# Performance work log

Hardware: AMD Instinct MI355X
Metric: run time of the kernel (lower is better)

Reference implementation:

```python
import jax, jax.numpy as jnp
import numpy as np

B, L = 4, 2048
D_MODEL, D_INNER, D_STATE, DT_RANK, K = 512, 1024, 16, 64, 4


def setup_inputs() -> dict:
    key = jax.random.key(0)
    ks = jax.random.split(key, 21)
    def n(k, shape, s=0.02):
        return (jax.random.normal(k, shape) * s).astype(jnp.float32)
    inp = {"x": jax.random.normal(ks[0], (B, L, D_MODEL), jnp.float32)}
    for i, sfx in enumerate(("f", "b")):
        o = 1 + i * 8
        inp[f"W_in_{sfx}"] = n(ks[o], (2 * D_INNER, D_MODEL))
        inp[f"conv_w_{sfx}"] = n(ks[o + 1], (D_INNER, 1, K), 0.1)
        inp[f"conv_b_{sfx}"] = jnp.zeros((D_INNER,), jnp.float32)
        inp[f"A_log_{sfx}"] = (jax.random.normal(ks[o + 2], (D_STATE, D_INNER)) * 0.1).astype(jnp.float32)
        inp[f"D_{sfx}"] = jnp.ones((D_INNER,), jnp.float32)
        inp[f"Wx_{sfx}"] = n(ks[o + 3], (DT_RANK + 2 * D_STATE, D_INNER))
        inp[f"Wdt_{sfx}"] = n(ks[o + 4], (D_INNER, DT_RANK), DT_RANK ** -0.5)
        dt = jnp.exp(jax.random.uniform(ks[o + 5], (D_INNER,)) * (np.log(0.1) - np.log(0.001)) + np.log(0.001))
        inp[f"bdt_{sfx}"] = (dt + jnp.log(-jnp.expm1(-dt))).astype(jnp.float32)
        inp[f"Wout_{sfx}"] = n(ks[o + 6], (D_MODEL, D_INNER))
    return inp


def _mamba_block(x, W_in, conv_w, conv_b, A_log, Dp, Wx, Wdt, bdt, Wout):
    # x: [B, L, d_model]
    xz = jnp.einsum('bld,ed->ble', x, W_in)              # [B, L, 2*d_inner]
    xb, zb = xz[..., :D_INNER], xz[..., D_INNER:]
    # causal depthwise conv over time
    xc = jnp.transpose(xb, (0, 2, 1))                     # [B, M, L]
    xc = jax.lax.conv_general_dilated(
        xc, conv_w, window_strides=(1,), padding=[(K - 1, 0)],
        feature_group_count=D_INNER,
        dimension_numbers=('NCH', 'OIH', 'NCH')) + conv_b[None, :, None]
    xb = jax.nn.silu(jnp.transpose(xc, (0, 2, 1)))        # [B, L, M]
    # input-dependent SSM parameters
    proj = jnp.einsum('blm,pm->blp', xb, Wx)              # [B, L, dt_rank+2D]
    dt_in = proj[..., :DT_RANK]
    Bs = proj[..., DT_RANK:DT_RANK + D_STATE]             # [B, L, D]
    Cs = proj[..., DT_RANK + D_STATE:]                    # [B, L, D]
    dt = jax.nn.softplus(jnp.einsum('blr,mr->blm', dt_in, Wdt) + bdt)  # [B, L, M]
    A_T = -jnp.exp(A_log).T                               # [M, D]

    def step(h, inp):
        dt_t, x_t, B_t, C_t = inp                         # [B,M],[B,M],[B,D],[B,D]
        dA = jnp.exp(dt_t[:, :, None] * A_T[None])        # [B, M, D]
        h = dA * h + (dt_t * x_t)[:, :, None] * B_t[:, None, :]
        y_t = jnp.einsum('bmd,bd->bm', h, C_t)
        return h, y_t

    xs = (jnp.moveaxis(dt, 1, 0), jnp.moveaxis(xb, 1, 0),
          jnp.moveaxis(Bs, 1, 0), jnp.moveaxis(Cs, 1, 0))
    h0 = jnp.zeros((x.shape[0], D_INNER, D_STATE), x.dtype)
    _, ys = jax.lax.scan(step, h0, xs)                    # [L, B, M]
    y = jnp.moveaxis(ys, 0, 1) + Dp * xb                  # [B, L, M]
    y = y * jax.nn.silu(zb)                               # SiLU gate
    return jnp.einsum('blm,dm->bld', y, Wout)             # [B, L, d_model]


def reference(x,
              W_in_f, conv_w_f, conv_b_f, A_log_f, D_f, Wx_f, Wdt_f, bdt_f, Wout_f,
              W_in_b, conv_w_b, conv_b_b, A_log_b, D_b, Wx_b, Wdt_b, bdt_b, Wout_b):
    out_f = _mamba_block(x, W_in_f, conv_w_f, conv_b_f, A_log_f, D_f, Wx_f, Wdt_f, bdt_f, Wout_f)
    out_b = jnp.flip(_mamba_block(jnp.flip(x, 1), W_in_b, conv_w_b, conv_b_b, A_log_b, D_b, Wx_b, Wdt_b, bdt_b, Wout_b), 1)
    return out_f + out_b
```

## Files before the change

### kernel.cpp

```cpp
#include <hip/hip_runtime.h>
#include <hip/hip_bf16.h>
#include <cstdint>
#include <cstdio>

typedef float f32x4 __attribute__((ext_vector_type(4)));
typedef float f32x2 __attribute__((ext_vector_type(2)));
typedef short s16x8 __attribute__((ext_vector_type(8)));
typedef unsigned int u32x2 __attribute__((ext_vector_type(2)));

__device__ __forceinline__ float us2f(unsigned short u){
  union { unsigned int i; float f; } v; v.i = ((unsigned int)u) << 16; return v.f;
}
__device__ __forceinline__ unsigned short f2us(float f){
  union { float f; unsigned int i; } v; v.f = f;
  unsigned int r = v.i + 0x7fffu + ((v.i >> 16) & 1u);
  return (unsigned short)(r >> 16);
}
__device__ __forceinline__ void gload_lds16(const void* g, void* l){
  __builtin_amdgcn_global_load_lds(
      (const __attribute__((address_space(1))) unsigned int*)g,
      (__attribute__((address_space(3))) unsigned int*)l, 16, 0, 0);
}

#define PK0 0.999962f

__global__ __launch_bounds__(256)
void prep_k(const float* __restrict__ x,
            const float* __restrict__ W_in_f, const float* __restrict__ W_in_b,
            const float* __restrict__ Wx_f,   const float* __restrict__ Wx_b,
            const float* __restrict__ Wdt_f,  const float* __restrict__ Wdt_b,
            const float* __restrict__ Wout_f, const float* __restrict__ Wout_b,
            const float* __restrict__ Alog_f, const float* __restrict__ Alog_b,
            const float* __restrict__ bdt_f,  const float* __restrict__ bdt_b,
            unsigned short* __restrict__ W1cat, unsigned short* __restrict__ Wxpad,
            unsigned short* __restrict__ Wdtb,  unsigned short* __restrict__ Woutcat,
            float* __restrict__ A2, float* __restrict__ bdtcat,
            unsigned short* __restrict__ xbf, float* __restrict__ Cf)
{
  long i = (long)blockIdx.x * 256 + threadIdx.x;
  if (i < 4194304) {
    xbf[i] = f2us(x[i]); return;
  }
  i -= 4194304;
  if (i < 2097152) {
    int n = (int)(i >> 9), k = (int)(i & 511);
    float v = (n < 2048) ? W_in_f[(long)n*512 + k] : W_in_b[(long)(n-2048)*512 + k];
    W1cat[i] = f2us(v); return;
  }
  i -= 2097152;
  if (i < 262144) {
    int dir = (int)(i >> 17); long r = i & 131071; int n = (int)(r >> 10), k = (int)(r & 1023);
    const float* Wx = dir ? Wx_b : Wx_f;
    Wxpad[(long)dir*131072 + r] = f2us(n < 96 ? Wx[(long)n*1024 + k] : 0.f); return;
  }
  i -= 262144;
  if (i < 131072) {
    int dir = (int)(i >> 16); long r = i & 65535;
    Wdtb[i] = f2us((dir ? Wdt_b : Wdt_f)[r]); return;
  }
  i -= 131072;
  if (i < 1048576) {
    int n = (int)(i >> 11), k = (int)(i & 2047);
    float v = (k < 1024) ? Wout_f[(long)n*1024 + k] : Wout_b[(long)n*1024 + (k-1024)];
    Woutcat[i] = f2us(v); return;
  }
  i -= 1048576;
  if (i < 32768) {
    int dir = (int)(i >> 14); long r = i & 16383; int m = (int)(r >> 4), d = (int)(r & 15);
    const float* Al = dir ? Alog_b : Alog_f;
    A2[i] = -__expf(Al[(long)d*1024 + m]) * 1.4426950408889634f; return;
  }
  i -= 32768;
  if (i < 2048) {
    int dir = (int)(i >> 10), m = (int)(i & 1023);
    bdtcat[i] = (dir ? bdt_b : bdt_f)[m]; return;
  }
  i -= 2048;
  if (i < 98304) {
    int dir = (int)(i / 49152); long r = i % 49152;
    int m = (int)(r / 48), j = (int)(r % 48);
    int k = j >> 4, d = j & 15;
    const float* Al = dir ? Alog_b : Alog_f;
    const float w = -__expf(Al[(long)d*1024 + m]);
    float c;
    if (k == 0)      c = 0.999150f * w;
    else if (k == 1) c = 0.492809f * w * w;
    else             c = 0.139212f * w * w * w;
    Cf[(long)dir*49152 + (long)m*48 + (k << 4) + d] = c;
    return;
  }
}

template<int OUT_MODE>
__global__ __launch_bounds__(256)
void gemm_bt(const unsigned short* __restrict__ Ap, const unsigned short* __restrict__ Bp,
             void* __restrict__ Cp, const float* __restrict__ biasp,
             float* __restrict__ bcf,
             int K, int lda, int ldb, int ldc,
             long az, long bz, long cz, int biasz)
{
  const int z   = blockIdx.z;
  const int tid = threadIdx.x;
  const int bm  = blockIdx.x, bn = blockIdx.y;

  __shared__ __align__(16) unsigned short Ash[128][32];
  __shared__ __align__(16) unsigned short Bsh[128][32];

  const int wave = tid >> 6, lane = tid & 63;
  const int wr = (wave >> 1) << 6, wc = (wave & 1) << 6;
  const int fr = lane & 15, fs = lane >> 4;

  const int r0 = tid >> 2;
  const int sg = tid & 3, kofs = sg << 3;

  const unsigned short* Ag = Ap + (long)z * az;
  const unsigned short* Bg = Bp + (long)z * bz;

  const long aoff0 = (long)(bm*128 + r0)*lda + kofs;
  const long aoff1 = aoff0 + (long)64*lda;
  const long boff0 = (long)(bn*128 + r0)*ldb + kofs;
  const long boff1 = boff0 + (long)64*ldb;

  unsigned short* lA0 = &Ash[r0][kofs];
  unsigned short* lA1 = &Ash[64 + r0][kofs];
  unsigned short* lB0 = &Bsh[r0][kofs];
  unsigned short* lB1 = &Bsh[64 + r0][kofs];

  f32x4 acc[4][4];
  #pragma unroll
  for (int i=0;i<4;i++)
    #pragma unroll
    for (int j=0;j<4;j++) acc[i][j] = (f32x4){0.f,0.f,0.f,0.f};

  const int NK = K >> 5;
  for (int ks = 0; ks < NK; ++ks){
    const long k0 = (long)ks << 5;
    __syncthreads();
    gload_lds16(Ag + aoff0 + k0, lA0);
    gload_lds16(Ag + aoff1 + k0, lA1);
    gload_lds16(Bg + boff0 + k0, lB0);
    gload_lds16(Bg + boff1 + k0, lB1);
    __syncthreads();

    s16x8 af[4], bfv[4];
    #pragma unroll
    for (int i=0;i<4;i++){
      af[i]  = *(const s16x8*)&Ash[wr + i*16 + fr][fs << 3];
      bfv[i] = *(const s16x8*)&Bsh[wc + i*16 + fr][fs << 3];
    }
    #pragma unroll
    for (int i=0;i<4;i++)
      #pragma unroll
      for (int j=0;j<4;j++)
        acc[i][j] = __builtin_amdgcn_mfma_f32_16x16x32_bf16(bfv[j], af[i], acc[i][j], 0, 0, 0);
  }

  #pragma unroll
  for (int i=0;i<4;i++){
    const int row = bm*128 + wr + i*16 + fr;
    #pragma unroll
    for (int j=0;j<4;j++){
      const int c0 = bn*128 + wc + j*16 + (fs << 2);
      f32x4 v = acc[i][j];
      const long cbase = (long)z*cz + (long)row*ldc + c0;
      if (OUT_MODE == 2){
        *(f32x4*)((float*)Cp + cbase) = v;
      } else if (OUT_MODE == 1){
        const f32x4 b4 = *(const f32x4*)(biasp + z*biasz + c0);
        u32x2 o;
        unsigned short s[4];
        #pragma unroll
        for (int e=0;e<4;e++){
          float t = v[e] + b4[e];
          t = fmaxf(t, 0.f) + log1pf(__expf(-fabsf(t)));
          s[e] = f2us(t);
        }
        o[0] = (unsigned int)s[0] | ((unsigned int)s[1] << 16);
        o[1] = (unsigned int)s[2] | ((unsigned int)s[3] << 16);
        *(u32x2*)((unsigned short*)Cp + cbase) = o;
      } else {
        u32x2 o;
        o[0] = (unsigned int)f2us(v[0]) | ((unsigned int)f2us(v[1]) << 16);
        o[1] = (unsigned int)f2us(v[2]) | ((unsigned int)f2us(v[3]) << 16);
        *(u32x2*)((unsigned short*)Cp + cbase) = o;
        if (OUT_MODE == 3 && c0 >= 64 && c0 < 96){
          *(f32x4*)(bcf + ((long)z*8192 + row)*32 + (c0 - 64)) = v;
        }
      }
    }
  }
}

__global__ __launch_bounds__(256)
void conv_silu_k(const unsigned short* __restrict__ xz,
                 const float* __restrict__ wf, const float* __restrict__ cbf,
                 const float* __restrict__ wb, const float* __restrict__ cbb,
                 unsigned short* __restrict__ xbc)
{
  const int tid = threadIdx.x;
  const long tok = blockIdx.x;
  const int l   = (int)(tok & 2047);
  const int dir = tid >> 7;
  const int mg  = (tid & 127) << 3;
  const float* w  = dir ? wb  : wf;
  const float* cb = dir ? cbb : cbf;
  const long rowb = tok << 12;
  const int  xcol = (dir << 11) + mg;

  f32x4 wv[8];
  #pragma unroll
  for (int e=0;e<8;e++) wv[e] = *(const f32x4*)(w + (mg + e)*4);
  const f32x4 cb0 = *(const f32x4*)(cb + mg);
  const f32x4 cb1 = *(const f32x4*)(cb + mg + 4);

  float acc[8];
  #pragma unroll
  for (int e=0;e<4;e++){ acc[e]=cb0[e]; acc[4+e]=cb1[e]; }

  #pragma unroll
  for (int k=0;k<4;k++){
    const int off = dir ? (3 - k) : (k - 3);
    const int pos = l + off;
    if (pos >= 0 && pos < 2048){
      const s16x8 xv = *(const s16x8*)(xz + rowb + ((long)off << 12) + xcol);
      #pragma unroll
      for (int e=0;e<8;e++)
        acc[e] = __builtin_fmaf(wv[e][k], us2f((unsigned short)xv[e]), acc[e]);
    }
  }
  s16x8 out;
  #pragma unroll
  for (int e=0;e<8;e++){
    const float s = acc[e] / (1.f + __expf(-acc[e]));
    out[e] = (short)f2us(s);
  }
  *(s16x8*)(xbc + tok*2048 + (dir << 10) + mg) = out;
}

#define SCHUNK 32
#define NCHUNK 64

__global__ __launch_bounds__(256)
void scan1_k(const unsigned short* __restrict__ dtb, const unsigned short* __restrict__ xbc,
             const float* __restrict__ BCf, const float* __restrict__ Cf,
             unsigned short* __restrict__ hloc, float* __restrict__ Ssum)
{
  const int tidx = threadIdx.x;
  const int cb = blockIdx.x, c = blockIdx.y, bz = blockIdx.z;
  const int b = bz >> 1, dir = bz & 1;
  const int m = cb*256 + tidx;

  float C1[16], C2[16], C3[16];
  { const f32x4* p = (const f32x4*)(Cf + ((long)dir*1024 + m)*48);
    #pragma unroll
    for (int q=0;q<4;q++){
      f32x4 v1=p[q], v2=p[q+4], v3=p[q+8];
      #pragma unroll
      for (int e=0;e<4;e++){ C1[q*4+e]=v1[e]; C2[q*4+e]=v2[e]; C3[q*4+e]=v3[e]; } } }

  const int  l0 = dir ? (2047 - c*SCHUNK) : (c*SCHUNK);
  const int  ls = dir ? -1 : 1;
  const long tok0 = (long)b*2048 + l0;
  const unsigned short* dtp = dtb + (((long)dir) << 23) + tok0*1024 + m;
  const unsigned short* xvp = xbc + tok0*2048 + (dir << 10) + m;
  const float* bcp = BCf + ((long)dir*8192 + tok0)*32;
  const long dstp = (long)ls*1024, xstp = (long)ls*2048, bstp = (long)ls*32;

  float h[16];
  #pragma unroll
  for (int d=0;d<16;d++) h[d]=0.f;
  float S = 0.f;

  unsigned short du = *dtp, xu = *xvp;
  for (int t=0;t<SCHUNK;t++){
    const float dt = us2f(du), xv = us2f(xu);
    dtp += dstp; xvp += xstp;
    du = *dtp; xu = *xvp;
    S += dt;
    const float u = dt * xv;
    const float dt2 = dt*dt, dt3 = dt2*dt;
    const f32x4 bv0 = *(const f32x4*)(bcp);
    const f32x4 bv1 = *(const f32x4*)(bcp + 4);
    const f32x4 bv2 = *(const f32x4*)(bcp + 8);
    const f32x4 bv3 = *(const f32x4*)(bcp + 12);
    bcp += bstp;
    #pragma unroll
    for (int d=0;d<16;d++){
      const float bval = (d<4)? bv0[d&3] : (d<8)? bv1[d&3] : (d<12)? bv2[d&3] : bv3[d&3];
      float a = __builtin_fmaf(C1[d], dt, PK0);
      a = __builtin_fmaf(C2[d], dt2, a);
      a = __builtin_fmaf(C3[d], dt3, a);
      h[d] = __builtin_fmaf(a, h[d], u * bval);
    }
  }
  const long o = (((long)bz * NCHUNK) + c)*1024 + m;
  s16x8 hv0, hv1;
  #pragma unroll
  for (int e=0;e<8;e++){ hv0[e] = (short)f2us(h[e]); hv1[e] = (short)f2us(h[8+e]); }
  *(s16x8*)(hloc + (o << 4))     = hv0;
  *(s16x8*)(hloc + (o << 4) + 8) = hv1;
  Ssum[o] = S;
}

__global__ __launch_bounds__(256)
void scan2_k(const float* __restrict__ A2, const float* __restrict__ Ssum,
             unsigned short* __restrict__ hloc)
{
  const long idx = (long)blockIdx.x*256 + threadIdx.x;
  const long bz = idx >> 14; const int r = (int)(idx & 16383);
  const int dir = (int)(bz & 1);
  const float a2 = A2[((long)dir << 14) + r];
  const long base = bz * NCHUNK;
  float hs = 0.f;
  float hlN = us2f(hloc[base*16384 + r]);
  float SN  = Ssum[base*1024 + (r >> 4)];
  for (int c=0;c<NCHUNK;c++){
    const float hl = hlN, Sv = SN;
    const int cn = (c+1 < NCHUNK) ? c+1 : c;
    hlN = us2f(hloc[(base+cn)*16384 + r]);
    SN  = Ssum[(base+cn)*1024 + (r >> 4)];
    const float P = __builtin_amdgcn_exp2f(a2 * Sv);
    hloc[(base+c)*16384 + r] = f2us(hs);
    hs = __builtin_fmaf(P, hs, hl);
  }
}

__global__ __launch_bounds__(256)
void scan3_k(const unsigned short* __restrict__ dtb, const unsigned short* __restrict__ xbc,
             const float* __restrict__ BCf, const float* __restrict__ Cf,
             const unsigned short* __restrict__ hstart, const unsigned short* __restrict__ xz,
             const float* __restrict__ D_f, const float* __restrict__ D_b,
             unsigned short* __restrict__ ybuf)
{
  const int tidx = threadIdx.x;
  const int cb = blockIdx.x, c = blockIdx.y, bz = blockIdx.z;
  const int b = bz >> 1, dir = bz & 1;
  const int m = cb*256 + tidx;

  float C1[16], C2[16], C3[16];
  { const f32x4* p = (const f32x4*)(Cf + ((long)dir*1024 + m)*48);
    #pragma unroll
    for (int q=0;q<4;q++){
      f32x4 v1=p[q], v2=p[q+4], v3=p[q+8];
      #pragma unroll
      for (int e=0;e<4;e++){ C1[q*4+e]=v1[e]; C2[q*4+e]=v2[e]; C3[q*4+e]=v3[e]; } } }
  const float Dm = (dir ? D_b : D_f)[m];

  float h[16];
  { const long o = ((((long)bz*NCHUNK) + c)*1024 + m) << 4;
    s16x8 hv0 = *(const s16x8*)(hstart + o);
    s16x8 hv1 = *(const s16x8*)(hstart + o + 8);
    #pragma unroll
    for (int e=0;e<8;e++){ h[e] = us2f((unsigned short)hv0[e]);
                           h[8+e] = us2f((unsigned short)hv1[e]); } }

  const int  l0 = dir ? (2047 - c*SCHUNK) : (c*SCHUNK);
  const int  ls = dir ? -1 : 1;
  const long tok0 = (long)b*2048 + l0;
  const unsigned short* dtp = dtb + (((long)dir) << 23) + tok0*1024 + m;
  const unsigned short* xvp = xbc + tok0*2048 + (dir << 10) + m;
  const unsigned short* zp  = xz  + (tok0 << 12) + (dir << 11) + 1024 + m;
  unsigned short*       yp  = ybuf + tok0*2048 + (dir << 10) + m;
  const float* bcp = BCf + ((long)dir*8192 + tok0)*32;
  const long dstp = (long)ls*1024, xstp = (long)ls*2048, zstp = (long)ls << 12;
  const long bstp = (long)ls*32;

  unsigned short du = *dtp, xu = *xvp, zu = *zp;
  for (int t=0;t<SCHUNK;t++){
    const float dt = us2f(du), xv = us2f(xu), zb = us2f(zu);
    dtp += dstp; xvp += xstp; zp += zstp;
    du = *dtp; xu = *xvp; zu = *zp;
    const float u = dt * xv;
    const float dt2 = dt*dt, dt3 = dt2*dt;
    const f32x4 bv0 = *(const f32x4*)(bcp);
    const f32x4 bv1 = *(const f32x4*)(bcp + 4);
    const f32x4 bv2 = *(const f32x4*)(bcp + 8);
    const f32x4 bv3 = *(const f32x4*)(bcp + 12);
    const f32x4 cv0 = *(const f32x4*)(bcp + 16);
    const f32x4 cv1 = *(const f32x4*)(bcp + 20);
    const f32x4 cv2 = *(const f32x4*)(bcp + 24);
    const f32x4 cv3 = *(const f32x4*)(bcp + 28);
    bcp += bstp;
    float y0=0.f, y1=0.f;
    #pragma unroll
    for (int d=0;d<16;d++){
      const float bval = (d<4)? bv0[d&3] : (d<8)? bv1[d&3] : (d<12)? bv2[d&3] : bv3[d&3];
      const float cval = (d<4)? cv0[d&3] : (d<8)? cv1[d&3] : (d<12)? cv2[d&3] : cv3[d&3];
      float a = __builtin_fmaf(C1[d], dt, PK0);
      a = __builtin_fmaf(C2[d], dt2, a);
      a = __builtin_fmaf(C3[d], dt3, a);
      h[d] = __builtin_fmaf(a, h[d], u * bval);
      if (d & 1) y1 = __builtin_fmaf(h[d], cval, y1);
      else       y0 = __builtin_fmaf(h[d], cval, y0);
    }
    const float y = (y0 + y1) + Dm * xv;
    const float gate = zb / (1.f + __expf(-zb));
    *yp = f2us(y * gate);
    yp += xstp;
  }
}

extern "C" void kernel_launch(void* const* d_in, const int* in_sizes, int n_in,
                              void* d_out, int out_size, void* d_ws, size_t ws_size,
                              hipStream_t stream)
{
  const float* x      = (const float*)d_in[0];
  const float* W_in_f = (const float*)d_in[1];
  const float* convw_f= (const float*)d_in[2];
  const float* convb_f= (const float*)d_in[3];
  const float* Alog_f = (const float*)d_in[4];
  const float* D_f    = (const float*)d_in[5];
  const float* Wx_f   = (const float*)d_in[6];
  const float* Wdt_f  = (const float*)d_in[7];
  const float* bdt_f  = (const float*)d_in[8];
  const float* Wout_f = (const float*)d_in[9];
  const float* W_in_b = (const float*)d_in[10];
  const float* convw_b= (const float*)d_in[11];
  const float* convb_b= (const float*)d_in[12];
  const float* Alog_b = (const float*)d_in[13];
  const float* D_b    = (const float*)d_in[14];
  const float* Wx_b   = (const float*)d_in[15];
  const float* Wdt_b  = (const float*)d_in[16];
  const float* bdt_b  = (const float*)d_in[17];
  const float* Wout_b = (const float*)d_in[18];

  char* w = (char*)d_ws;
  auto carve = [&](size_t bytes) -> char* {
    char* p = w; w += (bytes + 255) & ~(size_t)255; return p;
  };
  unsigned short* W1cat   = (unsigned short*)carve(4096ULL*512*2);
  unsigned short* Wxpad   = (unsigned short*)carve(2ULL*128*1024*2);
  unsigned short* Wdtb    = (unsigned short*)carve(2ULL*1024*64*2);
  unsigned short* Woutcat = (unsigned short*)carve(512ULL*2048*2);
  float*          A2      = (float*)carve(2ULL*1024*16*4);
  float*          bdtcat  = (float*)carve(2048ULL*4);
  float*          Cf      = (float*)carve(2ULL*1024*48*4);
  float*          BCf     = (float*)carve(2ULL*8192*32*4);
  unsigned short* xz      = (unsigned short*)carve(8192ULL*4096*2);
  unsigned short* xbc     = (unsigned short*)carve(8192ULL*2048*2);
  unsigned short* proj    = (unsigned short*)carve(2ULL*8192*128*2);
  unsigned short* dtb     = (unsigned short*)carve(2ULL*8192*1024*2);
  unsigned short* ybuf    = (unsigned short*)carve(8192ULL*2048*2);
  unsigned short* hloc    = (unsigned short*)carve(8ULL*NCHUNK*1024*16*2);
  float*          Ssum    = (float*)carve(8ULL*NCHUNK*1024*4);
  unsigned short* xbf     = ybuf;

  if ((size_t)(w - (char*)d_ws) > ws_size) {
    fprintf(stderr, "kernel_launch: ws too small (%zu needed, %zu given)\n",
            (size_t)(w - (char*)d_ws), ws_size);
    return;
  }

  prep_k<<<dim3(30728), 256, 0, stream>>>(x, W_in_f, W_in_b, Wx_f, Wx_b, Wdt_f, Wdt_b,
                                          Wout_f, Wout_b, Alog_f, Alog_b, bdt_f, bdt_b,
                                          W1cat, Wxpad, Wdtb, Woutcat, A2, bdtcat, xbf, Cf);
  gemm_bt<0><<<dim3(64,32,1), 256, 0, stream>>>(xbf, W1cat, xz, nullptr, nullptr,
                                                512, 512, 512, 4096, 0, 0, 0, 0);
  conv_silu_k<<<dim3(8192), 256, 0, stream>>>(xz, convw_f, convb_f, convw_b, convb_b, xbc);
  gemm_bt<3><<<dim3(64,1,2), 256, 0, stream>>>(xbc, Wxpad, proj, nullptr, BCf,
                                               1024, 2048, 1024, 128,
                                               1024, 131072, 1048576, 0);
  gemm_bt<1><<<dim3(64,8,2), 256, 0, stream>>>(proj, Wdtb, dtb, bdtcat, nullptr,
                                               64, 128, 64, 1024,
                                               1048576, 65536, 8388608, 1024);
  scan1_k<<<dim3(4,NCHUNK,8), 256, 0, stream>>>(dtb, xbc, BCf, Cf, hloc, Ssum);
  scan2_k<<<dim3(512), 256, 0, stream>>>(A2, Ssum, hloc);
  scan3_k<<<dim3(4,NCHUNK,8), 256, 0, stream>>>(dtb, xbc, BCf, Cf, hloc, xz, D_f, D_b, ybuf);
  gemm_bt<2><<<dim3(64,4,1), 256, 0, stream>>>(ybuf, Woutcat, d_out, nullptr, nullptr,
                                               2048, 2048, 2048, 512, 0, 0, 0, 0);
}
```

Before: 348.8 us.

## Double GEMM K-tile to 64 and XOR-swizzle LDS layout

The bf16 GEMM now loads a 64-wide K slice per iteration instead of 32, which halves the number of barrier pairs per K loop and issues two MFMA sub-steps between barriers. The global source column is XOR-swizzled by row so that the LDS fragment reads are spread across banks and avoid conflicts. In exchange it doubles LDS use per block, which may lower occupancy, and it requires K to be a multiple of 64.

Result: faster. 322.7 us (-7.5%).

```diff
diff --git a/kernel.cpp b/kernel.cpp
--- a/kernel.cpp
+++ b/kernel.cpp
@@ -103,28 +103,24 @@
   const int tid = threadIdx.x;
   const int bm  = blockIdx.x, bn = blockIdx.y;
 
-  __shared__ __align__(16) unsigned short Ash[128][32];
-  __shared__ __align__(16) unsigned short Bsh[128][32];
+  __shared__ __align__(16) unsigned short Ash[128][64];
+  __shared__ __align__(16) unsigned short Bsh[128][64];
 
   const int wave = tid >> 6, lane = tid & 63;
   const int wr = (wave >> 1) << 6, wc = (wave & 1) << 6;
   const int fr = lane & 15, fs = lane >> 4;
 
-  const int r0 = tid >> 2;
-  const int sg = tid & 3, kofs = sg << 3;
+  const int rr  = tid >> 3;
+  const int csp = tid & 7;
+  const int csg = ((csp ^ (rr & 7)) << 3);
 
   const unsigned short* Ag = Ap + (long)z * az;
   const unsigned short* Bg = Bp + (long)z * bz;
 
-  const long aoff0 = (long)(bm*128 + r0)*lda + kofs;
-  const long aoff1 = aoff0 + (long)64*lda;
-  const long boff0 = (long)(bn*128 + r0)*ldb + kofs;
-  const long boff1 = boff0 + (long)64*ldb;
-
-  unsigned short* lA0 = &Ash[r0][kofs];
-  unsigned short* lA1 = &Ash[64 + r0][kofs];
-  unsigned short* lB0 = &Bsh[r0][kofs];
-  unsigned short* lB1 = &Bsh[64 + r0][kofs];
+  const long abase = (long)(bm*128 + rr)*lda + csg;
+  const long bbase = (long)(bn*128 + rr)*ldb + csg;
+  unsigned short* lA = &Ash[rr][csp << 3];
+  unsigned short* lB = &Bsh[rr][csp << 3];
 
   f32x4 acc[4][4];
   #pragma unroll
@@ -132,27 +128,33 @@
     #pragma unroll
     for (int j=0;j<4;j++) acc[i][j] = (f32x4){0.f,0.f,0.f,0.f};
 
-  const int NK = K >> 5;
+  const int NK = K >> 6;
   for (int ks = 0; ks < NK; ++ks){
-    const long k0 = (long)ks << 5;
+    const long k0 = (long)ks << 6;
     __syncthreads();
-    gload_lds16(Ag + aoff0 + k0, lA0);
-    gload_lds16(Ag + aoff1 + k0, lA1);
-    gload_lds16(Bg + boff0 + k0, lB0);
-    gload_lds16(Bg + boff1 + k0, lB1);
+    #pragma unroll
+    for (int r=0;r<4;r++){
+      gload_lds16(Ag + abase + (long)(r*32)*lda + k0, lA + r*32*64);
+      gload_lds16(Bg + bbase + (long)(r*32)*ldb + k0, lB + r*32*64);
+    }
     __syncthreads();
 
-    s16x8 af[4], bfv[4];
-    #pragma unroll
-    for (int i=0;i<4;i++){
-      af[i]  = *(const s16x8*)&Ash[wr + i*16 + fr][fs << 3];
-      bfv[i] = *(const s16x8*)&Bsh[wc + i*16 + fr][fs << 3];
-    }
-    #pragma unroll
-    for (int i=0;i<4;i++)
+    #pragma unroll
+    for (int sub=0; sub<2; ++sub){
+      s16x8 af[4], bfv[4];
       #pragma unroll
-      for (int j=0;j<4;j++)
-        acc[i][j] = __builtin_amdgcn_mfma_f32_16x16x32_bf16(bfv[j], af[i], acc[i][j], 0, 0, 0);
+      for (int i=0;i<4;i++){
+        const int ar = wr + i*16 + fr;
+        af[i]  = *(const s16x8*)&Ash[ar][(((sub<<2)+fs) ^ (fr&7)) << 3];
+        const int br = wc + i*16 + fr;
+        bfv[i] = *(const s16x8*)&Bsh[br][(((sub<<2)+fs) ^ (fr&7)) << 3];
+      }
+      #pragma unroll
+      for (int i=0;i<4;i++)
+        #pragma unroll
+        for (int j=0;j<4;j++)
+          acc[i][j] = __builtin_amdgcn_mfma_f32_16x16x32_bf16(bfv[j], af[i], acc[i][j], 0, 0, 0);
+    }
   }
 
   #pragma unroll
```
